# Kernel tuning notes

Hardware: AMD Instinct MI355X
Metric: run time of the kernel (lower is better)

The kernel has to match this reference:

```python
import jax, jax.numpy as jnp
import numpy as np

B, CIN, L, H, D, A = 2, 512, 1024, 32, 64, 2048  # A = H*D = att_features
SCALE = 0.05


def setup_inputs() -> dict:
    key = jax.random.key(0)
    ks = jax.random.split(key, 11)
    x = jax.random.normal(ks[0], (B, CIN, L), jnp.float32)
    # Per-head 1x1 Conv1d projections stacked over heads: weight [H, D, CIN], bias [H, D]
    Wq = jax.random.normal(ks[1], (H, D, CIN), jnp.float32) * SCALE
    bq = jax.random.normal(ks[2], (H, D), jnp.float32) * SCALE
    Wk = jax.random.normal(ks[3], (H, D, CIN), jnp.float32) * SCALE
    bk = jax.random.normal(ks[4], (H, D), jnp.float32) * SCALE
    Wv = jax.random.normal(ks[5], (H, D, CIN), jnp.float32) * SCALE
    bv = jax.random.normal(ks[6], (H, D), jnp.float32) * SCALE
    # final_block: Conv1d(A,A,1) -> ReLU -> Conv1d(A,A,1)
    W1 = jax.random.normal(ks[7], (A, A), jnp.float32) * SCALE
    b1 = jax.random.normal(ks[8], (A,), jnp.float32) * SCALE
    W2 = jax.random.normal(ks[9], (A, A), jnp.float32) * SCALE
    b2 = jax.random.normal(ks[10], (A,), jnp.float32) * SCALE
    return {"x": x, "Wq": Wq, "bq": bq, "Wk": Wk, "bk": bk,
            "Wv": Wv, "bv": bv, "W1": W1, "b1": b1, "W2": W2, "b2": b2}


def reference(x, Wq, bq, Wk, bk, Wv, bv, W1, b1, W2, b2):
    # 1x1 conv projections for all heads at once: [B,H,D,L]
    q = jnp.einsum('hdc,bcl->bhdl', Wq, x) + bq[None, :, :, None]
    k = jnp.einsum('hdc,bcl->bhdl', Wk, x) + bk[None, :, :, None]
    v = jnp.einsum('hdc,bcl->bhdl', Wv, x) + bv[None, :, :, None]
    # att = bmm(q^T, k): att[b,h,l,m] = sum_d q[b,h,d,l] * k[b,h,d,m]
    att = jnp.einsum('bhdl,bhdm->bhlm', q, k)
    # relative distance bias s_rel[i,j] = -|i-j|
    idx = jnp.arange(L)
    s_rel = -jnp.abs(idx[:, None] - idx[None, :]).astype(x.dtype)  # [L,L]
    att_map = jax.nn.softmax((att + s_rel) / float(np.sqrt(D)), axis=-1)
    # post-softmax upper-triangular mask (torch.triu keeps i <= j)
    masked = jnp.triu(att_map)
    # bmm(value, masked_att): out[b,h,d,m] = sum_l v[b,h,d,l] * masked[b,h,l,m]
    o = jnp.einsum('bhdl,bhlm->bhdm', v, masked)
    # per-head ReLU then concat heads along channel dim -> [B, A, L]
    h = jax.nn.relu(o).reshape(B, H * D, L)
    # final_block: 1x1 conv -> ReLU -> 1x1 conv
    z = jax.nn.relu(jnp.einsum('oc,bcl->bol', W1, h) + b1[None, :, None])
    z = jnp.einsum('oc,bcl->bol', W2, z) + b2[None, :, None]
    return z
```

## Files before the change

### kernel.cpp

```cpp
#include <hip/hip_runtime.h>

#define L 1024
#define CIN 512
#define NH 32
#define DH 64
#define NB 2
#define AF 2048

typedef unsigned short u16;
typedef unsigned int u32;
typedef __attribute__((ext_vector_type(8))) short bfx8;
typedef __attribute__((ext_vector_type(4))) short bfx4;
typedef __attribute__((ext_vector_type(4))) float fx4;

struct __align__(8) us4 { u16 x, y, z, w; };

#define MFMA16 __builtin_amdgcn_mfma_f32_16x16x32_bf16
#define SBAR() __builtin_amdgcn_s_barrier()
#define SFENCE() __builtin_amdgcn_sched_barrier(0)
#define WAIT_VM(N) asm volatile("s_waitcnt vmcnt(" #N ")" ::: "memory")
#define WAIT_LGKM0() asm volatile("s_waitcnt lgkmcnt(0)" ::: "memory")

__device__ inline void gld16(const void* g, void* l) {
    __builtin_amdgcn_global_load_lds(
        (const __attribute__((address_space(1))) u32*)g,
        (__attribute__((address_space(3))) u32*)l, 16, 0, 0);
}

__device__ inline u16 f2b(float f) {
    union { float f; u32 u; } v; v.f = f;
    u32 u = v.u;
    return (u16)((u + 0x7fffu + ((u >> 16) & 1u)) >> 16);
}

__global__ __launch_bounds__(256) void prep(
    const float* __restrict__ x,
    const float* __restrict__ Wq, const float* __restrict__ Wk, const float* __restrict__ Wv,
    const float* __restrict__ W1, const float* __restrict__ W2,
    u16* __restrict__ xT, u16* __restrict__ Wqb, u16* __restrict__ Wkb,
    u16* __restrict__ Wvb, u16* __restrict__ W1b, u16* __restrict__ W2b)
{
    __shared__ u16 tile[64][68];
    const int z = blockIdx.z;
    const int t = threadIdx.x;
    if (z < 5) {
        const float* in; u16* out; int n4;
        switch (z) {
            case 0: in = Wq; out = Wqb; n4 = AF * CIN / 4; break;
            case 1: in = Wk; out = Wkb; n4 = AF * CIN / 4; break;
            case 2: in = Wv; out = Wvb; n4 = AF * CIN / 4; break;
            case 3: in = W1; out = W1b; n4 = AF * AF / 4; break;
            default: in = W2; out = W2b; n4 = AF * AF / 4; break;
        }
        int i = blockIdx.x * 256 + t;
        for (; i < n4; i += 512 * 256) {
            float4 v = ((const float4*)in)[i];
            us4 o = { f2b(v.x), f2b(v.y), f2b(v.z), f2b(v.w) };
            ((us4*)out)[i] = o;
        }
    } else {
        const int bid = blockIdx.x;
        if (bid >= 256) return;
        const int c0 = (bid & 7) * 64, l0 = ((bid >> 3) & 15) * 64, b = bid >> 7;
        const int tr = t >> 4, tc4 = (t & 15) * 4;
        #pragma unroll
        for (int p = 0; p < 4; ++p) {
            int c = p * 16 + tr;
            float4 v = *(const float4*)(x + ((size_t)(b * CIN + c0 + c)) * L + l0 + tc4);
            tile[c][tc4 + 0] = f2b(v.x); tile[c][tc4 + 1] = f2b(v.y);
            tile[c][tc4 + 2] = f2b(v.z); tile[c][tc4 + 3] = f2b(v.w);
        }
        __syncthreads();
        #pragma unroll
        for (int p = 0; p < 4; ++p) {
            int l = p * 16 + tr;
            us4 o = { tile[tc4 + 0][l], tile[tc4 + 1][l], tile[tc4 + 2][l], tile[tc4 + 3][l] };
            *(us4*)(xT + ((size_t)(b * L + l0 + l)) * CIN + c0 + tc4) = o;
        }
    }
}

template<int RELU, int CT_OUT, int NA>
__global__ __launch_bounds__(512) void gemm_bt(
    const u16* __restrict__ A0, const u16* __restrict__ A1, const u16* __restrict__ A2,
    const float* __restrict__ bias0, const float* __restrict__ bias1, const float* __restrict__ bias2,
    const u16* __restrict__ BTb, void* __restrict__ Cb, void* __restrict__ Cb2,
    int M, int N, int K, size_t sBT, size_t sC, size_t sWhich)
{
    const int z = blockIdx.z;
    const int which = (NA == 3) ? (z % 3) : 0;
    const int b     = (NA == 3) ? (z / 3) : z;
    const u16* __restrict__ A = (which == 0) ? A0 : (which == 1) ? A1 : A2;
    const float* __restrict__ bias = (which == 0) ? bias0 : (which == 1) ? bias1 : bias2;
    const u16* __restrict__ BT = BTb + (size_t)b * sBT;

    const int lin  = blockIdx.x + (blockIdx.y << 3);
    const int lin2 = ((lin & 7) << 4) + (lin >> 3);
    const int m0 = (lin2 >> 3) * 128;
    const int n0 = (lin2 & 7) * 128;

    __shared__ u16 lA[2][4][128 * 32];
    __shared__ u16 lB[2][4][128 * 32];

    const int t = threadIdx.x, lane = t & 63, wave = t >> 6;
    const int grp = wave >> 2, wv = wave & 3;
    const int wm = (wv >> 1) * 64, wn = (wv & 1) * 64;
    const int rl = lane & 15, kh = lane >> 4;
    const int K2 = K >> 1;
    const int NT = K2 >> 5;

    fx4 acc[4][4];
    #pragma unroll
    for (int i = 0; i < 4; ++i)
        #pragma unroll
        for (int j = 0; j < 4; ++j) acc[i][j] = (fx4){0.f, 0.f, 0.f, 0.f};

    const int tt = t & 255;
    const int s0 = tt, s1 = tt + 256;
    const int r0 = s0 >> 2, cs0 = (s0 & 3) ^ ((r0 >> 1) & 3);
    const int r1 = s1 >> 2, cs1 = (s1 & 3) ^ ((r1 >> 1) & 3);
    const u16* gA0 = A  + (size_t)(m0 + r0) * K + grp * K2 + cs0 * 8;
    const u16* gA1 = A  + (size_t)(m0 + r1) * K + grp * K2 + cs1 * 8;
    const u16* gB0 = BT + (size_t)(n0 + r0) * K + grp * K2 + cs0 * 8;
    const u16* gB1 = BT + (size_t)(n0 + r1) * K + grp * K2 + cs1 * 8;

    int aoff[4], boff[4];
    #pragma unroll
    for (int f = 0; f < 4; ++f) {
        int ra = wm + f * 16 + rl;
        int rb = wn + f * 16 + rl;
        aoff[f] = ra * 32 + ((kh ^ ((ra >> 1) & 3)) * 8);
        boff[f] = rb * 32 + ((kh ^ ((rb >> 1) & 3)) * 8);
    }

#define STAGE(BF, K0) do { \
        gld16(gA0 + (K0), &lA[grp][BF][s0 * 8]); \
        gld16(gA1 + (K0), &lA[grp][BF][s1 * 8]); \
        gld16(gB0 + (K0), &lB[grp][BF][s0 * 8]); \
        gld16(gB1 + (K0), &lB[grp][BF][s1 * 8]); } while (0)

    STAGE(0, 0); STAGE(1, 32); STAGE(2, 64);

    for (int it = 0; it < NT; ++it) {
        if (it + 2 < NT) {
            WAIT_VM(8);
        } else if (it + 1 < NT) {
            WAIT_VM(4);
        } else {
            WAIT_VM(0);
        }
        SBAR(); SFENCE();
        if (it + 3 < NT) STAGE((it + 3) & 3, (it + 3) << 5);
        const u16* bA = &lA[grp][it & 3][0];
        const u16* bB = &lB[grp][it & 3][0];
        bfx8 af[4], bfr[4];
        #pragma unroll
        for (int f = 0; f < 4; ++f) af[f] = *(const bfx8*)&bA[aoff[f]];
        #pragma unroll
        for (int f = 0; f < 4; ++f) bfr[f] = *(const bfx8*)&bB[boff[f]];
        __builtin_amdgcn_s_setprio(1);
        #pragma unroll
        for (int fm = 0; fm < 4; ++fm)
            #pragma unroll
            for (int fn = 0; fn < 4; ++fn)
                acc[fm][fn] = MFMA16(af[fm], bfr[fn], acc[fm][fn], 0, 0, 0);
        __builtin_amdgcn_s_setprio(0);
    }
#undef STAGE

    __syncthreads();
    float* red = (float*)&lA[0][0][0];
    if (grp == 1) {
        #pragma unroll
        for (int fm = 0; fm < 4; ++fm)
            #pragma unroll
            for (int fn = 0; fn < 4; ++fn)
                *(fx4*)&red[(((wv * 16 + fm * 4 + fn) * 64) + lane) * 4] = acc[fm][fn];
    }
    __syncthreads();
    if (grp != 0) return;
    #pragma unroll
    for (int fm = 0; fm < 4; ++fm)
        #pragma unroll
        for (int fn = 0; fn < 4; ++fn) {
            fx4 p = *(const fx4*)&red[(((wv * 16 + fm * 4 + fn) * 64) + lane) * 4];
            acc[fm][fn] += p;
        }

    if (NA == 3 && which == 2) {
        u16* Vn = (u16*)Cb2 + (size_t)b * (size_t)M * N;
        #pragma unroll
        for (int fm = 0; fm < 4; ++fm) {
            int mg = m0 + wm + fm * 16 + kh * 4;
            #pragma unroll
            for (int fn = 0; fn < 4; ++fn) {
                int ng = n0 + wn + fn * 16 + rl;
                #pragma unroll
                for (int r = 0; r < 4; ++r)
                    Vn[(size_t)(mg + r) * N + ng] = f2b(acc[fm][fn][r] + bias[mg + r]);
            }
        }
    } else if (CT_OUT) {
        const float sc = (NA == 3 && which == 0) ? 0.125f : 1.0f;
        u16* CT = (u16*)Cb + (size_t)which * sWhich + (size_t)b * sC;
        #pragma unroll
        for (int fm = 0; fm < 4; ++fm) {
            int mg = m0 + wm + fm * 16 + kh * 4;
            float bi0 = bias[mg], bi1 = bias[mg + 1], bi2 = bias[mg + 2], bi3 = bias[mg + 3];
            #pragma unroll
            for (int fn = 0; fn < 4; ++fn) {
                int ng = n0 + wn + fn * 16 + rl;
                float v0 = (acc[fm][fn][0] + bi0) * sc;
                float v1 = (acc[fm][fn][1] + bi1) * sc;
                float v2 = (acc[fm][fn][2] + bi2) * sc;
                float v3 = (acc[fm][fn][3] + bi3) * sc;
                if (RELU) {
                    v0 = fmaxf(v0, 0.f); v1 = fmaxf(v1, 0.f);
                    v2 = fmaxf(v2, 0.f); v3 = fmaxf(v3, 0.f);
                }
                us4 o = { f2b(v0), f2b(v1), f2b(v2), f2b(v3) };
                *(us4*)(CT + (size_t)ng * M + mg) = o;
            }
        }
    } else {
        float* C = (float*)Cb + (size_t)b * sC;
        #pragma unroll
        for (int fm = 0; fm < 4; ++fm) {
            int mg = m0 + wm + fm * 16 + kh * 4;
            #pragma unroll
            for (int fn = 0; fn < 4; ++fn) {
                int ng = n0 + wn + fn * 16 + rl;
                #pragma unroll
                for (int r = 0; r < 4; ++r) {
                    float v = acc[fm][fn][r] + bias[mg + r];
                    if (RELU) v = fmaxf(v, 0.f);
                    C[(size_t)(mg + r) * N + ng] = v;
                }
            }
        }
    }
}

__global__ __launch_bounds__(256) void attn_stats(
    const u16* __restrict__ qT, const u16* __restrict__ kT,
    float* __restrict__ rinv)
{
    const int lt = blockIdx.x;
    const int bh = blockIdx.y;
    const int b = bh >> 5, h = bh & 31;
    const size_t base = (size_t)b * L * AF + h * DH;

    const int mlo = lt < 2 ? 0 : lt - 2;
    const int mhi = lt > 13 ? 15 : lt + 2;
    const int NTW = mhi - mlo + 1;

    __shared__ u16 lq[64 * 64];
    __shared__ u16 lk[4][64 * 64];
    __shared__ float sS[4][64];

    const int t = threadIdx.x, lane = t & 63, wave = t >> 6;
    const int rl = lane & 15, g = lane >> 4;

    const int s0 = t, s1 = t + 256;
    const int r0 = s0 >> 3, cs0 = (s0 & 7) ^ (r0 & 7);
    const int r1 = s1 >> 3, cs1 = (s1 & 7) ^ (r1 & 7);

    const u16* gk0 = kT + base + (size_t)(mlo * 64 + r0) * AF + cs0 * 8;
    const u16* gk1 = kT + base + (size_t)(mlo * 64 + r1) * AF + cs1 * 8;

    gld16(qT + base + (size_t)(lt * 64 + r0) * AF + cs0 * 8, lq + s0 * 8);
    gld16(qT + base + (size_t)(lt * 64 + r1) * AF + cs1 * 8, lq + s1 * 8);
    gld16(gk0, &lk[0][s0 * 8]);
    gld16(gk1, &lk[0][s1 * 8]);
    gld16(gk0 + (size_t)64 * AF, &lk[1][s0 * 8]);
    gld16(gk1 + (size_t)64 * AF, &lk[1][s1 * 8]);
    WAIT_VM(2); SBAR(); SFENCE();

    const int rmr = wave * 16 + rl;
    const int akoff0 = rmr * 64 + ((g ^ (rmr & 7)) * 8);
    const int akoff1 = rmr * 64 + (((g + 4) ^ (rmr & 7)) * 8);
    bfx8 qf0[4], qf1[4];
    #pragma unroll
    for (int f = 0; f < 4; ++f) {
        int rq = f * 16 + rl;
        qf0[f] = *(const bfx8*)&lq[rq * 64 + ((g ^ (rq & 7)) * 8)];
        qf1[f] = *(const bfx8*)&lq[rq * 64 + (((g + 4) ^ (rq & 7)) * 8)];
    }

    float Sx[4] = {0.f, 0.f, 0.f, 0.f};
    for (int i = 0; i < NTW; ++i) {
        if (i + 2 < NTW) {
            const int bf = (i + 2) & 3;
            gld16(gk0 + (size_t)(i + 2) * 64 * AF, &lk[bf][s0 * 8]);
            gld16(gk1 + (size_t)(i + 2) * 64 * AF, &lk[bf][s1 * 8]);
            WAIT_VM(4);
        } else if (i + 1 < NTW) {
            WAIT_VM(2);
        } else {
            WAIT_VM(0);
        }
        SBAR(); SFENCE();
        const u16* kb = lk[i & 3];
        bfx8 ak0 = *(const bfx8*)&kb[akoff0];
        bfx8 ak1 = *(const bfx8*)&kb[akoff1];
        const float mb = (float)((mlo + i) * 64 + wave * 16 + g * 4);
        #pragma unroll
        for (int fn = 0; fn < 4; ++fn) {
            fx4 att = (fx4){0.f, 0.f, 0.f, 0.f};
            att = MFMA16(ak0, qf0[fn], att, 0, 0, 0);
            att = MFMA16(ak1, qf1[fn], att, 0, 0, 0);
            const float lgf = (float)(lt * 64 + fn * 16 + rl);
            float e0 = __expf(att[0] - 0.125f * fabsf(lgf - mb));
            float e1 = __expf(att[1] - 0.125f * fabsf(lgf - (mb + 1.f)));
            float e2 = __expf(att[2] - 0.125f * fabsf(lgf - (mb + 2.f)));
            float e3 = __expf(att[3] - 0.125f * fabsf(lgf - (mb + 3.f)));
            Sx[fn] += (e0 + e1) + (e2 + e3);
        }
    }
    #pragma unroll
    for (int fn = 0; fn < 4; ++fn) {
        float s_ = Sx[fn];
        s_ += __shfl_xor(s_, 16);
        s_ += __shfl_xor(s_, 32);
        if (lane < 16) sS[wave][fn * 16 + rl] = s_;
    }
    __syncthreads();
    if (t < 64) {
        float s_ = sS[0][t] + sS[1][t] + sS[2][t] + sS[3][t];
        rinv[(size_t)bh * L + lt * 64 + t] = 1.0f / s_;
    }
}

__global__ __launch_bounds__(256) void attn_pv(
    const u16* __restrict__ qT, const u16* __restrict__ kT, const u16* __restrict__ v,
    const float* __restrict__ rinv, u16* __restrict__ hT)
{
    const int mt = blockIdx.x;
    const int bh = blockIdx.y;
    const int b = bh >> 5, h = bh & 31;
    const size_t qkbase = (size_t)b * L * AF + h * DH;
    const size_t vbase  = ((size_t)b * AF + h * DH) * L;
    const size_t rbase  = (size_t)bh * L;

    const int ltlo = mt < 2 ? 0 : mt - 2;
    const int NI = mt - ltlo + 1;
    const int m0 = mt * 64;

    __shared__ u16 lkt[64 * 64];
    __shared__ u16 lqt[2][64 * 64], lv[2][64 * 64];
    __shared__ u16 lw[64 * 68];

    const int t = threadIdx.x, lane = t & 63, wave = t >> 6;
    const int rl = lane & 15, g = lane >> 4;

    const int s0 = t, s1 = t + 256;
    const int r0 = s0 >> 3, cs0 = (s0 & 7) ^ (r0 & 7);
    const int r1 = s1 >> 3, cs1 = (s1 & 7) ^ (r1 & 7);

    const u16* gq0 = qT + qkbase + (size_t)(ltlo * 64 + r0) * AF + cs0 * 8;
    const u16* gq1 = qT + qkbase + (size_t)(ltlo * 64 + r1) * AF + cs1 * 8;
    const u16* gv0 = v + vbase + ltlo * 64 + (size_t)r0 * L + cs0 * 8;
    const u16* gv1 = v + vbase + ltlo * 64 + (size_t)r1 * L + cs1 * 8;

    const int rmr = wave * 16 + rl;
    const int toff0 = rmr * 64 + ((g ^ (rmr & 7)) * 8);
    const int toff1 = rmr * 64 + (((g + 4) ^ (rmr & 7)) * 8);
    int qoff0[4], qoff1[4];
    #pragma unroll
    for (int f = 0; f < 4; ++f) {
        int rq = f * 16 + rl;
        qoff0[f] = rq * 64 + ((g ^ (rq & 7)) * 8);
        qoff1[f] = rq * 64 + (((g + 4) ^ (rq & 7)) * 8);
    }

    gld16(kT + qkbase + (size_t)(m0 + r0) * AF + cs0 * 8, lkt + s0 * 8);
    gld16(kT + qkbase + (size_t)(m0 + r1) * AF + cs1 * 8, lkt + s1 * 8);
    gld16(gq0, &lqt[0][s0 * 8]);
    gld16(gq1, &lqt[0][s1 * 8]);
    gld16(gv0, &lv[0][s0 * 8]);
    gld16(gv1, &lv[0][s1 * 8]);
    WAIT_VM(0); SBAR(); SFENCE();

    fx4 oa[4];
    #pragma unroll
    for (int f = 0; f < 4; ++f) oa[f] = (fx4){0.f, 0.f, 0.f, 0.f};

    int cur = 0;
    for (int i = 0; i < NI; ++i) {
        const int lt = ltlo + i;
        if (i + 1 < NI) {
            gld16(gq0 + (size_t)(i + 1) * 64 * AF, &lqt[cur ^ 1][s0 * 8]);
            gld16(gq1 + (size_t)(i + 1) * 64 * AF, &lqt[cur ^ 1][s1 * 8]);
            gld16(gv0 + (i + 1) * 64, &lv[cur ^ 1][s0 * 8]);
            gld16(gv1 + (i + 1) * 64, &lv[cur ^ 1][s1 * 8]);
        }
        bfx8 ak0 = *(const bfx8*)&lkt[toff0];
        bfx8 ak1 = *(const bfx8*)&lkt[toff1];
        const u16* qb = lqt[cur];
        #pragma unroll
        for (int fn = 0; fn < 4; ++fn) {
            bfx8 q0 = *(const bfx8*)&qb[qoff0[fn]];
            bfx8 q1 = *(const bfx8*)&qb[qoff1[fn]];
            fx4 att = (fx4){0.f, 0.f, 0.f, 0.f};
            att = MFMA16(ak0, q0, att, 0, 0, 0);
            att = MFMA16(ak1, q1, att, 0, 0, 0);
            const int lg = lt * 64 + fn * 16 + rl;
            float ri = rinv[rbase + lg];
            const float db = (float)(lg - (m0 + wave * 16 + g * 4));
            #pragma unroll
            for (int r = 0; r < 4; ++r) {
                int mloc = wave * 16 + g * 4 + r;
                float s = att[r] - 0.125f * fabsf(db - (float)r);
                float w = (lg <= m0 + mloc) ? __expf(s) * ri : 0.f;
                lw[mloc * 68 + fn * 16 + rl] = f2b(w);
            }
        }
        WAIT_LGKM0(); SBAR(); SFENCE();

        const u16* vb = lv[cur];
        bfx8 av0 = *(const bfx8*)&vb[toff0];
        bfx8 av1 = *(const bfx8*)&vb[toff1];
        #pragma unroll
        for (int fn = 0; fn < 4; ++fn) {
            const u16* wrow = &lw[(fn * 16 + rl) * 68];
            union { bfx8 f; bfx4 hh[2]; } w0, w1;
            w0.hh[0] = *(const bfx4*)&wrow[g * 8];
            w0.hh[1] = *(const bfx4*)&wrow[g * 8 + 4];
            w1.hh[0] = *(const bfx4*)&wrow[(g + 4) * 8];
            w1.hh[1] = *(const bfx4*)&wrow[(g + 4) * 8 + 4];
            oa[fn] = MFMA16(av0, w0.f, oa[fn], 0, 0, 0);
            oa[fn] = MFMA16(av1, w1.f, oa[fn], 0, 0, 0);
        }
        WAIT_VM(0); WAIT_LGKM0(); SBAR(); SFENCE();
        cur ^= 1;
    }

    #pragma unroll
    for (int fn = 0; fn < 4; ++fn) {
        int mg = m0 + fn * 16 + rl;
        int cg = h * DH + wave * 16 + g * 4;
        us4 o = { f2b(fmaxf(oa[fn][0], 0.f)), f2b(fmaxf(oa[fn][1], 0.f)),
                  f2b(fmaxf(oa[fn][2], 0.f)), f2b(fmaxf(oa[fn][3], 0.f)) };
        *(us4*)(hT + ((size_t)b * L + mg) * AF + cg) = o;
    }
}

extern "C" void kernel_launch(void* const* d_in, const int* in_sizes, int n_in,
                              void* d_out, int out_size, void* d_ws, size_t ws_size,
                              hipStream_t stream)
{
    (void)in_sizes; (void)n_in; (void)out_size; (void)ws_size;
    const float* x  = (const float*)d_in[0];
    const float* Wq = (const float*)d_in[1];
    const float* bq = (const float*)d_in[2];
    const float* Wk = (const float*)d_in[3];
    const float* bk = (const float*)d_in[4];
    const float* Wv = (const float*)d_in[5];
    const float* bv = (const float*)d_in[6];
    const float* W1 = (const float*)d_in[7];
    const float* b1 = (const float*)d_in[8];
    const float* W2 = (const float*)d_in[9];
    const float* b2 = (const float*)d_in[10];

    u16* wsp = (u16*)d_ws;
    size_t o = 0;
    u16* xT  = wsp + o; o += (size_t)NB * L * CIN;
    u16* qT  = wsp + o; o += (size_t)NB * L * AF;
    u16* kT  = wsp + o; o += (size_t)NB * L * AF;
    u16* vdm = wsp + o; o += (size_t)NB * AF * L;
    u16* hT  = wsp + o; o += (size_t)NB * L * AF;
    u16* z1T = wsp + o; o += (size_t)NB * L * AF;
    u16* Wqb = wsp + o; o += (size_t)AF * CIN;
    u16* Wkb = wsp + o; o += (size_t)AF * CIN;
    u16* Wvb = wsp + o; o += (size_t)AF * CIN;
    u16* W1b = wsp + o; o += (size_t)AF * AF;
    u16* W2b = wsp + o; o += (size_t)AF * AF;
    float* rinv = (float*)(wsp + o); o += (size_t)NB * NH * L * 2;

    dim3 blk(256);
    dim3 blk5(512);

    prep<<<dim3(512, 1, 6), blk, 0, stream>>>(x, Wq, Wk, Wv, W1, W2,
                                              xT, Wqb, Wkb, Wvb, W1b, W2b);

    gemm_bt<0, 1, 3><<<dim3(8, 16, NB * 3), blk5, 0, stream>>>(
        Wqb, Wkb, Wvb, bq, bk, bv, xT, qT, vdm,
        AF, L, CIN, (size_t)L * CIN, (size_t)L * AF, (size_t)NB * L * AF);

    attn_stats<<<dim3(16, NB * NH), blk, 0, stream>>>(qT, kT, rinv);
    attn_pv<<<dim3(16, NB * NH), blk, 0, stream>>>(qT, kT, vdm, rinv, hT);

    gemm_bt<1, 1, 1><<<dim3(8, 16, NB), blk5, 0, stream>>>(
        W1b, nullptr, nullptr, b1, nullptr, nullptr, hT, z1T, nullptr,
        AF, L, AF, (size_t)L * AF, (size_t)L * AF, 0);
    gemm_bt<0, 0, 1><<<dim3(8, 16, NB), blk5, 0, stream>>>(
        W2b, nullptr, nullptr, b2, nullptr, nullptr, z1T, d_out, nullptr,
        AF, L, AF, (size_t)L * AF, (size_t)AF * L, 0);
}
```

Before: 146.9 us.

## Shrink GEMM blocks to four waves with 128x64 per-wave tiles

The split-K GEMM now launches 256 threads (two K-groups of two waves) instead of 512, and each wave computes a 128x64 output tile with 8x4 MFMA fragments instead of 64x64. Each thread issues four async global-to-LDS loads per operand per stage instead of two, and the vmcnt waits are doubled to match. The goal is fewer waves competing for the same LDS tiles and more MFMA work per LDS fragment load. In exchange, each wave holds twice as many accumulators and A fragments, which raises register pressure, and the kernel has fewer waves per block to hide latency.

```diff
diff --git a/kernel.cpp b/kernel.cpp
--- a/kernel.cpp
+++ b/kernel.cpp
@@ -81,7 +81,7 @@
 }
 
 template<int RELU, int CT_OUT, int NA>
-__global__ __launch_bounds__(512) void gemm_bt(
+__global__ __launch_bounds__(256) void gemm_bt(
     const u16* __restrict__ A0, const u16* __restrict__ A1, const u16* __restrict__ A2,
     const float* __restrict__ bias0, const float* __restrict__ bias1, const float* __restrict__ bias2,
     const u16* __restrict__ BTb, void* __restrict__ Cb, void* __restrict__ Cb2,
@@ -103,64 +103,72 @@
     __shared__ u16 lB[2][4][128 * 32];
 
     const int t = threadIdx.x, lane = t & 63, wave = t >> 6;
-    const int grp = wave >> 2, wv = wave & 3;
-    const int wm = (wv >> 1) * 64, wn = (wv & 1) * 64;
+    const int grp = wave >> 1, cw = wave & 1;
     const int rl = lane & 15, kh = lane >> 4;
     const int K2 = K >> 1;
     const int NT = K2 >> 5;
 
-    fx4 acc[4][4];
-    #pragma unroll
-    for (int i = 0; i < 4; ++i)
+    fx4 acc[8][4];
+    #pragma unroll
+    for (int i = 0; i < 8; ++i)
         #pragma unroll
         for (int j = 0; j < 4; ++j) acc[i][j] = (fx4){0.f, 0.f, 0.f, 0.f};
 
-    const int tt = t & 255;
-    const int s0 = tt, s1 = tt + 256;
-    const int r0 = s0 >> 2, cs0 = (s0 & 3) ^ ((r0 >> 1) & 3);
-    const int r1 = s1 >> 2, cs1 = (s1 & 3) ^ ((r1 >> 1) & 3);
-    const u16* gA0 = A  + (size_t)(m0 + r0) * K + grp * K2 + cs0 * 8;
-    const u16* gA1 = A  + (size_t)(m0 + r1) * K + grp * K2 + cs1 * 8;
-    const u16* gB0 = BT + (size_t)(n0 + r0) * K + grp * K2 + cs0 * 8;
-    const u16* gB1 = BT + (size_t)(n0 + r1) * K + grp * K2 + cs1 * 8;
-
-    int aoff[4], boff[4];
+    const int tt = t & 127;
+    const u16* gAp[4];
+    const u16* gBp[4];
+    int sdst[4];
+    #pragma unroll
+    for (int i = 0; i < 4; ++i) {
+        int s = tt + i * 128;
+        int row = s >> 2;
+        int col = (s & 3) ^ ((row >> 1) & 3);
+        sdst[i] = s * 8;
+        gAp[i] = A  + (size_t)(m0 + row) * K + grp * K2 + col * 8;
+        gBp[i] = BT + (size_t)(n0 + row) * K + grp * K2 + col * 8;
+    }
+
+    int aoff[8], boff[4];
+    #pragma unroll
+    for (int f = 0; f < 8; ++f) {
+        int ra = f * 16 + rl;
+        aoff[f] = ra * 32 + ((kh ^ ((ra >> 1) & 3)) * 8);
+    }
     #pragma unroll
     for (int f = 0; f < 4; ++f) {
-        int ra = wm + f * 16 + rl;
-        int rb = wn + f * 16 + rl;
-        aoff[f] = ra * 32 + ((kh ^ ((ra >> 1) & 3)) * 8);
+        int rb = cw * 64 + f * 16 + rl;
         boff[f] = rb * 32 + ((kh ^ ((rb >> 1) & 3)) * 8);
     }
 
 #define STAGE(BF, K0) do { \
-        gld16(gA0 + (K0), &lA[grp][BF][s0 * 8]); \
-        gld16(gA1 + (K0), &lA[grp][BF][s1 * 8]); \
-        gld16(gB0 + (K0), &lB[grp][BF][s0 * 8]); \
-        gld16(gB1 + (K0), &lB[grp][BF][s1 * 8]); } while (0)
+        gld16(gAp[0] + (K0), &lA[grp][BF][sdst[0]]); \
+        gld16(gAp[1] + (K0), &lA[grp][BF][sdst[1]]); \
+        gld16(gAp[2] + (K0), &lA[grp][BF][sdst[2]]); \
+        gld16(gAp[3] + (K0), &lA[grp][BF][sdst[3]]); \
+        gld16(gBp[0] + (K0), &lB[grp][BF][sdst[0]]); \
+        gld16(gBp[1] + (K0), &lB[grp][BF][sdst[1]]); \
+        gld16(gBp[2] + (K0), &lB[grp][BF][sdst[2]]); \
+        gld16(gBp[3] + (K0), &lB[grp][BF][sdst[3]]); } while (0)
 
     STAGE(0, 0); STAGE(1, 32); STAGE(2, 64);
 
     for (int it = 0; it < NT; ++it) {
-        if (it + 2 < NT) {
-            WAIT_VM(8);
-        } else if (it + 1 < NT) {
-            WAIT_VM(4);
-        } else {
-            WAIT_VM(0);
-        }
+        const int rem = NT - 1 - it;
+        if (rem >= 2) { WAIT_VM(16); }
+        else if (rem == 1) { WAIT_VM(8); }
+        else { WAIT_VM(0); }
         SBAR(); SFENCE();
         if (it + 3 < NT) STAGE((it + 3) & 3, (it + 3) << 5);
         const u16* bA = &lA[grp][it & 3][0];
         const u16* bB = &lB[grp][it & 3][0];
-        bfx8 af[4], bfr[4];
-        #pragma unroll
-        for (int f = 0; f < 4; ++f) af[f] = *(const bfx8*)&bA[aoff[f]];
+        bfx8 af[8], bfr[4];
+        #pragma unroll
+        for (int f = 0; f < 8; ++f) af[f] = *(const bfx8*)&bA[aoff[f]];
         #pragma unroll
         for (int f = 0; f < 4; ++f) bfr[f] = *(const bfx8*)&bB[boff[f]];
         __builtin_amdgcn_s_setprio(1);
         #pragma unroll
-        for (int fm = 0; fm < 4; ++fm)
+        for (int fm = 0; fm < 8; ++fm)
             #pragma unroll
             for (int fn = 0; fn < 4; ++fn)
                 acc[fm][fn] = MFMA16(af[fm], bfr[fn], acc[fm][fn], 0, 0, 0);
@@ -172,29 +180,29 @@
     float* red = (float*)&lA[0][0][0];
     if (grp == 1) {
         #pragma unroll
-        for (int fm = 0; fm < 4; ++fm)
+        for (int fm = 0; fm < 8; ++fm)
             #pragma unroll
             for (int fn = 0; fn < 4; ++fn)
-                *(fx4*)&red[(((wv * 16 + fm * 4 + fn) * 64) + lane) * 4] = acc[fm][fn];
+                *(fx4*)&red[(((cw * 32 + fm * 4 + fn) * 64) + lane) * 4] = acc[fm][fn];
     }
     __syncthreads();
     if (grp != 0) return;
     #pragma unroll
-    for (int fm = 0; fm < 4; ++fm)
+    for (int fm = 0; fm < 8; ++fm)
         #pragma unroll
         for (int fn = 0; fn < 4; ++fn) {
-            fx4 p = *(const fx4*)&red[(((wv * 16 + fm * 4 + fn) * 64) + lane) * 4];
+            fx4 p = *(const fx4*)&red[(((cw * 32 + fm * 4 + fn) * 64) + lane) * 4];
             acc[fm][fn] += p;
         }
 
     if (NA == 3 && which == 2) {
         u16* Vn = (u16*)Cb2 + (size_t)b * (size_t)M * N;
         #pragma unroll
-        for (int fm = 0; fm < 4; ++fm) {
-            int mg = m0 + wm + fm * 16 + kh * 4;
+        for (int fm = 0; fm < 8; ++fm) {
+            int mg = m0 + fm * 16 + kh * 4;
             #pragma unroll
             for (int fn = 0; fn < 4; ++fn) {
-                int ng = n0 + wn + fn * 16 + rl;
+                int ng = n0 + cw * 64 + fn * 16 + rl;
                 #pragma unroll
                 for (int r = 0; r < 4; ++r)
                     Vn[(size_t)(mg + r) * N + ng] = f2b(acc[fm][fn][r] + bias[mg + r]);
@@ -204,12 +212,12 @@
         const float sc = (NA == 3 && which == 0) ? 0.125f : 1.0f;
         u16* CT = (u16*)Cb + (size_t)which * sWhich + (size_t)b * sC;
         #pragma unroll
-        for (int fm = 0; fm < 4; ++fm) {
-            int mg = m0 + wm + fm * 16 + kh * 4;
+        for (int fm = 0; fm < 8; ++fm) {
+            int mg = m0 + fm * 16 + kh * 4;
             float bi0 = bias[mg], bi1 = bias[mg + 1], bi2 = bias[mg + 2], bi3 = bias[mg + 3];
             #pragma unroll
             for (int fn = 0; fn < 4; ++fn) {
-                int ng = n0 + wn + fn * 16 + rl;
+                int ng = n0 + cw * 64 + fn * 16 + rl;
                 float v0 = (acc[fm][fn][0] + bi0) * sc;
                 float v1 = (acc[fm][fn][1] + bi1) * sc;
                 float v2 = (acc[fm][fn][2] + bi2) * sc;
@@ -225,11 +233,11 @@
     } else {
         float* C = (float*)Cb + (size_t)b * sC;
         #pragma unroll
-        for (int fm = 0; fm < 4; ++fm) {
-            int mg = m0 + wm + fm * 16 + kh * 4;
+        for (int fm = 0; fm < 8; ++fm) {
+            int mg = m0 + fm * 16 + kh * 4;
             #pragma unroll
             for (int fn = 0; fn < 4; ++fn) {
-                int ng = n0 + wn + fn * 16 + rl;
+                int ng = n0 + cw * 64 + fn * 16 + rl;
                 #pragma unroll
                 for (int r = 0; r < 4; ++r) {
                     float v = acc[fm][fn][r] + bias[mg + r];
@@ -478,22 +486,21 @@
     float* rinv = (float*)(wsp + o); o += (size_t)NB * NH * L * 2;
 
     dim3 blk(256);
-    dim3 blk5(512);
 
     prep<<<dim3(512, 1, 6), blk, 0, stream>>>(x, Wq, Wk, Wv, W1, W2,
                                               xT, Wqb, Wkb, Wvb, W1b, W2b);
 
-    gemm_bt<0, 1, 3><<<dim3(8, 16, NB * 3), blk5, 0, stream>>>(
+    gemm_bt<0, 1, 3><<<dim3(8, 16, NB * 3), blk, 0, stream>>>(
         Wqb, Wkb, Wvb, bq, bk, bv, xT, qT, vdm,
         AF, L, CIN, (size_t)L * CIN, (size_t)L * AF, (size_t)NB * L * AF);
 
     attn_stats<<<dim3(16, NB * NH), blk, 0, stream>>>(qT, kT, rinv);
     attn_pv<<<dim3(16, NB * NH), blk, 0, stream>>>(qT, kT, vdm, rinv, hT);
 
-    gemm_bt<1, 1, 1><<<dim3(8, 16, NB), blk5, 0, stream>>>(
+    gemm_bt<1, 1, 1><<<dim3(8, 16, NB), blk, 0, stream>>>(
         W1b, nullptr, nullptr, b1, nullptr, nullptr, hT, z1T, nullptr,
         AF, L, AF, (size_t)L * AF, (size_t)L * AF, 0);
-    gemm_bt<0, 0, 1><<<dim3(8, 16, NB), blk5, 0, stream>>>(
+    gemm_bt<0, 0, 1><<<dim3(8, 16, NB), blk, 0, stream>>>(
         W2b, nullptr, nullptr, b2, nullptr, nullptr, z1T, d_out, nullptr,
         AF, L, AF, (size_t)L * AF, (size_t)AF * L, 0);
 }
```

After: 166.2 us. 1.13x slower.
